# Kernel tuning notes

Measured on AMD Instinct MI355X. Metric: run time of the kernel, lower is better.

Reference implementation:

```python
import jax, jax.numpy as jnp
import numpy as np

D_MODEL = 512
D_STATE = 128
D_CONV = 4
EXPAND = 2
HEADDIM = 64
D_INNER = EXPAND * D_MODEL            # 1024
NHEADS = D_INNER // HEADDIM           # 16
CONV_DIM = D_INNER + 2 * D_STATE      # 1280
D_IN_PROJ = 2 * D_INNER + 2 * D_STATE + NHEADS  # 2320
EPS = 1e-5


def _mamba2(u, in_w, conv_w, conv_b, A_log, dt_bias, Dp, norm_w, out_w):
    # u: [b, l, d_model]  -- Mamba2 forward (ngroups=1), SSD in exact quadratic form
    b, l, _ = u.shape
    zxbcdt = u @ in_w.T                                   # [b,l,2320]
    z = zxbcdt[..., :D_INNER]
    xBC = zxbcdt[..., D_INNER:D_INNER + CONV_DIM]
    dt = zxbcdt[..., D_INNER + CONV_DIM:]                 # [b,l,nheads]
    # causal depthwise conv1d (kernel 4) + silu
    xp = jnp.pad(xBC, ((0, 0), (D_CONV - 1, 0), (0, 0)))
    conv = sum(xp[:, k:k + l, :] * conv_w[:, k] for k in range(D_CONV))
    xBC = jax.nn.silu(conv + conv_b)
    x = xBC[..., :D_INNER].reshape(b, l, NHEADS, HEADDIM)
    Bm = xBC[..., D_INNER:D_INNER + D_STATE]              # [b,l,d_state]
    Cm = xBC[..., D_INNER + D_STATE:]                     # [b,l,d_state]
    dt = jax.nn.softplus(dt + dt_bias)                    # [b,l,nheads]
    dtA = dt * (-jnp.exp(A_log))                          # [b,l,nheads], negative
    # SSD quadratic (semiseparable) form: L[t,s] = exp(sum_{r=s+1..t} dtA_r), causal
    cs = jnp.cumsum(dtA, axis=1)                          # [b,l,nh]
    seg = cs[:, :, None, :] - cs[:, None, :, :]           # [b,t,s,nh]
    mask = jnp.tril(jnp.ones((l, l), bool))
    L = jnp.exp(jnp.where(mask[None, :, :, None], seg, -jnp.inf))
    G = jnp.einsum('btd,bsd->bts', Cm, Bm)                # C_t . B_s
    dtx = dt[..., None] * x                               # [b,l,nh,hd]
    y = jnp.einsum('btsn,bsnp->btnp', G[..., None] * L, dtx)
    y = (y + x * Dp[:, None]).reshape(b, l, D_INNER)      # D skip
    # gated RMSNorm (norm_before_gate=False): rmsnorm(y * silu(z)) * weight
    y = y * jax.nn.silu(z)
    y = y * jax.lax.rsqrt(jnp.mean(jnp.square(y), -1, keepdims=True) + EPS) * norm_w
    return y @ out_w.T


def _forward(x, h_in_w, h_conv_w, h_conv_b, h_A_log, h_dt_bias, h_D, h_norm_w, h_out_w,
             v_in_w, v_conv_w, v_conv_b, v_A_log, v_dt_bias, v_D, v_norm_w, v_out_w,
             fc_w, fc_b):
    B, H, W, C = x.shape
    hp = (h_in_w, h_conv_w, h_conv_b, h_A_log, h_dt_bias, h_D, h_norm_w, h_out_w)
    vp = (v_in_w, v_conv_w, v_conv_b, v_A_log, v_dt_bias, v_D, v_norm_w, v_out_w)
    # horizontal: scan along W for each (B*H) row
    xh = x.reshape(-1, W, C)
    h1 = _mamba2(xh, *hp)
    # NOTE: original code flips dim 0 (batch), reproduced faithfully
    h2 = jnp.flip(_mamba2(jnp.flip(xh, 0), *hp), 0)
    h = jnp.concatenate([h1, h2], -1).reshape(B, H, W, -1)
    # vertical: scan along H for each (B*W) column
    xv = jnp.transpose(x, (0, 2, 1, 3)).reshape(-1, H, C)
    v1 = _mamba2(xv, *vp)
    v2 = jnp.flip(_mamba2(jnp.flip(xv, 0), *vp), 0)
    v = jnp.transpose(jnp.concatenate([v1, v2], -1).reshape(B, W, H, -1), (0, 2, 1, 3))
    out = jnp.concatenate([v, h], -1) @ fc_w.T + fc_b     # [B,H,W,C]
    return out


def setup_inputs() -> dict:
    key = jax.random.key(0)
    ks = jax.random.split(key, 8)
    B, H, W, C = 2, 64, 64, D_MODEL
    x = jax.random.normal(ks[0], (B, H, W, C), jnp.float32)

    def mk(k):
        kk = jax.random.split(k, 5)
        return {
            'in_w': 0.02 * jax.random.normal(kk[0], (D_IN_PROJ, D_MODEL), jnp.float32),
            'conv_w': 0.1 * jax.random.normal(kk[1], (CONV_DIM, D_CONV), jnp.float32),
            'conv_b': jnp.zeros((CONV_DIM,), jnp.float32),
            'A_log': jnp.log(jax.random.uniform(kk[2], (NHEADS,), jnp.float32, 1.0, 16.0)),
            'dt_bias': jnp.log(jnp.expm1(jax.random.uniform(kk[3], (NHEADS,), jnp.float32, 1e-3, 0.1))),
            'D': jnp.ones((NHEADS,), jnp.float32),
            'norm_w': jnp.ones((D_INNER,), jnp.float32),
            'out_w': 0.02 * jax.random.normal(kk[4], (D_MODEL, D_INNER), jnp.float32),
        }

    hp, vp = mk(ks[1]), mk(ks[2])
    inp = {'x': x}
    inp.update({f'h_{n}': v for n, v in hp.items()})
    inp.update({f'v_{n}': v for n, v in vp.items()})
    inp['fc_w'] = 0.02 * jax.random.normal(ks[3], (D_MODEL, 4 * D_MODEL), jnp.float32)
    inp['fc_b'] = jnp.zeros((D_MODEL,), jnp.float32)
    return inp


def reference(x, h_in_w, h_conv_w, h_conv_b, h_A_log, h_dt_bias, h_D, h_norm_w, h_out_w,
              v_in_w, v_conv_w, v_conv_b, v_A_log, v_dt_bias, v_D, v_norm_w, v_out_w,
              fc_w, fc_b):
    return _forward(x, h_in_w, h_conv_w, h_conv_b, h_A_log, h_dt_bias, h_D, h_norm_w, h_out_w,
                    v_in_w, v_conv_w, v_conv_b, v_A_log, v_dt_bias, v_D, v_norm_w, v_out_w,
                    fc_w, fc_b)
```

## Files before the change

### kernel.cpp

```cpp
#include <hip/hip_runtime.h>

#define NROWS 8192
#define NZX   2304
#define BCS   136
#define XMS   72

typedef __attribute__((ext_vector_type(8))) short bf16x8;
typedef __attribute__((ext_vector_type(4))) float f32x4;

__device__ __forceinline__ float bf2f(unsigned short u) {
    union { unsigned int i; float f; } v; v.i = ((unsigned int)u) << 16; return v.f;
}
__device__ __forceinline__ unsigned short f2bf(float f) {
    union { float f; unsigned int i; } v; v.f = f;
    unsigned int r = v.i + 0x7FFFu + ((v.i >> 16) & 1u);
    return (unsigned short)(r >> 16);
}

__device__ __forceinline__ void async_lds16(const unsigned short* g, unsigned short* l) {
    __builtin_amdgcn_global_load_lds(
        (const __attribute__((address_space(1))) unsigned int*)g,
        (__attribute__((address_space(3))) unsigned int*)l, 16, 0, 0);
}

__global__ void cvt_bf16(const float* __restrict__ s, unsigned short* __restrict__ d, int n4)
{
    int i = blockIdx.x * 256 + threadIdx.x;
    if (i >= n4) return;
    float4 v = *(const float4*)(s + (size_t)i * 4);
    ushort4 o;
    o.x = f2bf(v.x); o.y = f2bf(v.y); o.z = f2bf(v.z); o.w = f2bf(v.w);
    *(ushort4*)(d + (size_t)i * 4) = o;
}

__global__ void cvt2_bf16(const float* __restrict__ s0, const float* __restrict__ s1,
                          unsigned short* __restrict__ d, int n4)
{
    int i = blockIdx.x * 256 + threadIdx.x;
    if (i >= n4) return;
    const float* s = blockIdx.y ? s1 : s0;
    float4 v = *(const float4*)(s + (size_t)i * 4);
    ushort4 o;
    o.x = f2bf(v.x); o.y = f2bf(v.y); o.z = f2bf(v.z); o.w = f2bf(v.w);
    *(ushort4*)(d + (size_t)blockIdx.y * (2304 * 512) + (size_t)i * 4) = o;
}

__global__ __launch_bounds__(256) void cvtT_bf16(
    const float* __restrict__ s0, const float* __restrict__ s1,
    unsigned short* __restrict__ d0, unsigned short* __restrict__ d1)
{
    __shared__ float T[64][65];
    const float* s = blockIdx.z ? s1 : s0;
    unsigned short* d = blockIdx.z ? d1 : d0;
    const int tid = threadIdx.x;
    const int bo = blockIdx.x * 64, bc = blockIdx.y * 64;
#pragma unroll
    for (int i = 0; i < 16; ++i) {
        int slot = tid + i * 256;
        int r = slot >> 6, c = slot & 63;
        T[r][c] = s[(size_t)(bo + r) * 1024 + bc + c];
    }
    __syncthreads();
#pragma unroll
    for (int i = 0; i < 16; ++i) {
        int slot = tid + i * 256;
        int cr = slot >> 6, oc = slot & 63;
        d[(size_t)(bc + cr) * 512 + bo + oc] = f2bf(T[oc][cr]);
    }
}

__global__ __launch_bounds__(256) void gemm128_btz(
    const unsigned short* __restrict__ A0, const unsigned short* __restrict__ A1,
    const unsigned short* __restrict__ B0, const unsigned short* __restrict__ B1,
    unsigned short* __restrict__ C0, unsigned short* __restrict__ C1,
    int K, int lda, int ldb, int ldc, int permflag)
{
    __shared__ unsigned short As[128 * 32];
    __shared__ unsigned short Bs[128 * 32];
    const int z = blockIdx.z;
    const unsigned short* A = z ? A1 : A0;
    const unsigned short* B = z ? B1 : B0;
    unsigned short* C = z ? C1 : C0;
    const int perm = permflag & z;
    const int tid = threadIdx.x, wave = tid >> 6, lane = tid & 63;
    const int mB = blockIdx.x * 128, nB = blockIdx.y * 128;
    const int wm = (wave >> 1) * 64, wn = (wave & 1) * 64;
    const int lr = lane & 15, lq = lane >> 4;
    const int s0 = wave * 64 + lane, s1 = s0 + 256;
    const int row0 = s0 >> 2, q0 = (s0 & 3) ^ ((row0 >> 1) & 3);
    const int row1 = s1 >> 2, q1 = (s1 & 3) ^ ((row1 >> 1) & 3);
    int ar0 = mB + row0, ar1 = mB + row1;
    if (perm) {
        ar0 = (ar0 & ~4095) | ((ar0 & 63) << 6) | ((ar0 >> 6) & 63);
        ar1 = (ar1 & ~4095) | ((ar1 & 63) << 6) | ((ar1 >> 6) & 63);
    }
    const unsigned short* Ag0 = A + (size_t)ar0 * lda + q0 * 8;
    const unsigned short* Ag1 = A + (size_t)ar1 * lda + q1 * 8;
    const unsigned short* Bg0 = B + (size_t)(nB + row0) * ldb + q0 * 8;
    const unsigned short* Bg1 = B + (size_t)(nB + row1) * ldb + q1 * 8;
    unsigned short* lA0 = As + s0 * 8; unsigned short* lA1 = As + s1 * 8;
    unsigned short* lB0 = Bs + s0 * 8; unsigned short* lB1 = Bs + s1 * 8;
    const int sw = (lq ^ ((lr >> 1) & 3)) * 8;
    int aoff[4], boff[4];
#pragma unroll
    for (int i = 0; i < 4; ++i) {
        aoff[i] = (wm + i * 16 + lr) * 32 + sw;
        boff[i] = (wn + i * 16 + lr) * 32 + sw;
    }
    f32x4 zero4 = {0.f,0.f,0.f,0.f};
    f32x4 acc[4][4] = {{zero4,zero4,zero4,zero4},{zero4,zero4,zero4,zero4},
                       {zero4,zero4,zero4,zero4},{zero4,zero4,zero4,zero4}};
    for (int k0 = 0; k0 < K; k0 += 32) {
        async_lds16(Ag0 + k0, lA0);
        async_lds16(Ag1 + k0, lA1);
        async_lds16(Bg0 + k0, lB0);
        async_lds16(Bg1 + k0, lB1);
        __syncthreads();
        bf16x8 a[4], b[4];
#pragma unroll
        for (int i = 0; i < 4; ++i) a[i] = *(const bf16x8*)(As + aoff[i]);
#pragma unroll
        for (int i = 0; i < 4; ++i) b[i] = *(const bf16x8*)(Bs + boff[i]);
#pragma unroll
        for (int mi = 0; mi < 4; ++mi)
#pragma unroll
            for (int ni = 0; ni < 4; ++ni)
                acc[mi][ni] = __builtin_amdgcn_mfma_f32_16x16x32_bf16(
                    a[mi], b[ni], acc[mi][ni], 0, 0, 0);
        __syncthreads();
    }
    const int rbase = lq * 4;
#pragma unroll
    for (int mi = 0; mi < 4; ++mi)
#pragma unroll
        for (int ni = 0; ni < 4; ++ni) {
            int col = nB + wn + ni * 16 + lr;
#pragma unroll
            for (int r = 0; r < 4; ++r) {
                int row = mB + wm + mi * 16 + rbase + r;
                C[(size_t)row * ldc + col] = f2bf(acc[mi][ni][r]);
            }
        }
}

__global__ __launch_bounds__(256) void gemm_final2048(
    const unsigned short* __restrict__ YV, const unsigned short* __restrict__ YH,
    const unsigned short* __restrict__ W, const float* __restrict__ bias,
    float* __restrict__ C)
{
    __shared__ unsigned short As[128 * 32];
    __shared__ unsigned short Bs[64 * 32];
    const int tid = threadIdx.x, wave = tid >> 6, lane = tid & 63;
    const int mB = blockIdx.x * 128, nB = blockIdx.y * 64;
    const int lr = lane & 15, lq = lane >> 4;
    const int sA0 = tid, sA1 = tid + 256;
    const int rA0 = sA0 >> 2, qA0 = ((sA0 & 3) ^ ((rA0 >> 1) & 3)) * 8;
    const int rA1 = sA1 >> 2, qA1 = ((sA1 & 3) ^ ((rA1 >> 1) & 3)) * 8;
    const int rB  = tid >> 2, qB  = ((tid & 3) ^ ((rB >> 1) & 3)) * 8;
    const int g0r = mB + rA0, g1r = mB + rA1;
    const int p0r = (g0r & ~4095) | ((g0r & 63) << 6) | ((g0r >> 6) & 63);
    const int p1r = (g1r & ~4095) | ((g1r & 63) << 6) | ((g1r >> 6) & 63);
    const unsigned short* Bg = W + (size_t)(nB + rB) * 2048 + qB;
    unsigned short* lA0 = As + sA0 * 8; unsigned short* lA1 = As + sA1 * 8;
    unsigned short* lB  = Bs + tid * 8;
    const int sw = (lq ^ ((lr >> 1) & 3)) * 8;
    int aoff[2], boff[4];
#pragma unroll
    for (int i = 0; i < 2; ++i) aoff[i] = (wave * 32 + i * 16 + lr) * 32 + sw;
#pragma unroll
    for (int i = 0; i < 4; ++i) boff[i] = (i * 16 + lr) * 32 + sw;
    f32x4 zero4 = {0.f,0.f,0.f,0.f};
    f32x4 acc[2][4] = {{zero4,zero4,zero4,zero4},{zero4,zero4,zero4,zero4}};
    for (int k0 = 0; k0 < 2048; k0 += 32) {
        int kk0 = k0 + qA0, kk1 = k0 + qA1;
        const unsigned short* g0 = (kk0 < 1024) ? YV + (size_t)p0r * 1024 + kk0
                                                : YH + (size_t)g0r * 1024 + (kk0 - 1024);
        const unsigned short* g1 = (kk1 < 1024) ? YV + (size_t)p1r * 1024 + kk1
                                                : YH + (size_t)g1r * 1024 + (kk1 - 1024);
        async_lds16(g0, lA0);
        async_lds16(g1, lA1);
        async_lds16(Bg + k0, lB);
        __syncthreads();
        bf16x8 a[2], b[4];
#pragma unroll
        for (int i = 0; i < 2; ++i) a[i] = *(const bf16x8*)(As + aoff[i]);
#pragma unroll
        for (int i = 0; i < 4; ++i) b[i] = *(const bf16x8*)(Bs + boff[i]);
#pragma unroll
        for (int mi = 0; mi < 2; ++mi)
#pragma unroll
            for (int ni = 0; ni < 4; ++ni)
                acc[mi][ni] = __builtin_amdgcn_mfma_f32_16x16x32_bf16(
                    a[mi], b[ni], acc[mi][ni], 0, 0, 0);
        __syncthreads();
    }
    const int rbase = lq * 4;
#pragma unroll
    for (int mi = 0; mi < 2; ++mi)
#pragma unroll
        for (int ni = 0; ni < 4; ++ni) {
            int col = nB + ni * 16 + lr;
            float bb = bias[col];
#pragma unroll
            for (int r = 0; r < 4; ++r) {
                int row = mB + wave * 32 + mi * 16 + rbase + r;
                C[(size_t)row * 512 + col] = acc[mi][ni][r] + bb;
            }
        }
}

__global__ __launch_bounds__(320) void conv_silu(
    const unsigned short* __restrict__ zxb, const float* __restrict__ cw0,
    const float* __restrict__ cw1, const float* __restrict__ cb0,
    const float* __restrict__ cb1, unsigned short* __restrict__ xbcb)
{
    __shared__ unsigned short S[64 * 320];
    const int dir = blockIdx.y;
    const unsigned short* zx = zxb + (size_t)dir * NROWS * NZX;
    unsigned short* xbc = xbcb + (size_t)dir * NROWS * 1280;
    const float* cw = dir ? cw1 : cw0;
    const float* cb = dir ? cb1 : cb0;
    const int tid = threadIdx.x;
    const int seq = blockIdx.x >> 2, tile = blockIdx.x & 3;
    const int cbase = tile * 320;
    const unsigned short* src = zx + (size_t)seq * 64 * NZX + 1024 + cbase;
#pragma unroll
    for (int i = 0; i < 8; ++i) {
        int slot = tid + i * 320;
        int r = slot / 40, ch = (slot % 40) * 8;
        *(uint4*)(S + r * 320 + ch) = *(const uint4*)(src + (size_t)r * NZX + ch);
    }
    __syncthreads();
    const int c8 = (tid % 40) * 8, rg = tid / 40;
    const int gc = cbase + c8;
    float4 b0 = *(const float4*)(cb + gc), b1 = *(const float4*)(cb + gc + 4);
    const float bias[8] = {b0.x,b0.y,b0.z,b0.w,b1.x,b1.y,b1.z,b1.w};
    float4 wv[8];
#pragma unroll
    for (int j = 0; j < 8; ++j) wv[j] = *(const float4*)(cw + (size_t)(gc + j) * 4);
    unsigned short* dst = xbc + (size_t)seq * 64 * 1280 + gc;
#pragma unroll
    for (int r = 0; r < 8; ++r) {
        int t = rg * 8 + r;
        float acc[8];
#pragma unroll
        for (int j = 0; j < 8; ++j) acc[j] = bias[j];
#pragma unroll
        for (int k = 0; k < 4; ++k) {
            int ts = t + k - 3;
            if (ts >= 0) {
                uint4 xv = *(const uint4*)(S + ts * 320 + c8);
                const unsigned short* xs = (const unsigned short*)&xv;
#pragma unroll
                for (int j = 0; j < 8; ++j)
                    acc[j] += bf2f(xs[j]) * ((const float*)&wv[j])[k];
            }
        }
        unsigned short out8[8] __attribute__((aligned(16)));
#pragma unroll
        for (int j = 0; j < 8; ++j) out8[j] = f2bf(acc[j] / (1.f + __expf(-acc[j])));
        *(uint4*)(dst + (size_t)t * 1280) = *(const uint4*)out8;
    }
}

__global__ __launch_bounds__(256) void dt_cs(
    const float* __restrict__ x, const float* __restrict__ iw0,
    const float* __restrict__ iw1, const float* __restrict__ db0,
    const float* __restrict__ db1, const float* __restrict__ al0,
    const float* __restrict__ al1, float* __restrict__ dtbb,
    float* __restrict__ csbb)
{
    __shared__ float wsm[4][512];
    __shared__ float xs[64][68];
    __shared__ float dta[4][64], dtt[4][64];
    const int dir = blockIdx.y;
    const float* in_w = dir ? iw1 : iw0;
    const float* dt_bias = dir ? db1 : db0;
    const float* A_log = dir ? al1 : al0;
    float* dtb = dtbb + (size_t)dir * 131072;
    float* csb = csbb + (size_t)dir * 131072;
    const int tid = threadIdx.x;
    const int seq = blockIdx.x >> 2, hq = blockIdx.x & 3;
#pragma unroll
    for (int i = 0; i < 2; ++i) {
        int slot = tid + i * 256;
        int h = slot >> 7, c = (slot & 127) * 4;
        *(float4*)&wsm[h][c] = *(const float4*)(in_w + (size_t)(2304 + hq * 4 + h) * 512 + c);
    }
    const int t = tid & 63, hh = tid >> 6;
    const int h = hq * 4 + hh;
    float acc = 0.f;
    for (int c0 = 0; c0 < 512; c0 += 64) {
        __syncthreads();
#pragma unroll
        for (int i = 0; i < 4; ++i) {
            int slot = tid + i * 256;
            int r = slot >> 4, cc = (slot & 15) * 4;
            size_t row = (dir == 0) ? (size_t)seq * 64 + r
                                    : (size_t)(seq >> 6) * 4096 + (size_t)r * 64 + (seq & 63);
            *(float4*)&xs[r][cc] = *(const float4*)(x + row * 512 + c0 + cc);
        }
        __syncthreads();
#pragma unroll
        for (int cc = 0; cc < 64; cc += 4) {
            float4 u4 = *(const float4*)&xs[t][cc];
            const float* w = &wsm[hh][c0 + cc];
            acc += u4.x * w[0] + u4.y * w[1] + u4.z * w[2] + u4.w * w[3];
        }
    }
    float v = acc + dt_bias[h];
    float dtv = (v > 20.f) ? v : log1pf(__expf(v));
    dtt[hh][t] = dtv;
    dta[hh][t] = dtv * -__expf(A_log[h]);
    __syncthreads();
    if (tid < 4) {
        float run = 0.f;
        int ob = (seq * 16 + hq * 4 + tid) * 64;
        for (int tt = 0; tt < 64; ++tt) {
            run += dta[tid][tt];
            dtb[ob + tt] = dtt[tid][tt];
            csb[ob + tt] = run;
        }
    }
}

__global__ __launch_bounds__(256) void scan_kernel(
    const unsigned short* __restrict__ xbcb, const float* __restrict__ dtbb,
    const float* __restrict__ csbb, const float* __restrict__ Dv0,
    const float* __restrict__ Dv1, unsigned short* __restrict__ yh,
    unsigned short* __restrict__ yv)
{
    __shared__ unsigned short Bs[64 * BCS];
    __shared__ unsigned short Cs[64 * BCS];
    __shared__ unsigned short XsT[64 * XMS];
    __shared__ unsigned short Ms[64 * XMS];
    __shared__ float dts[64], css[64];
    const int dir = blockIdx.y;
    const unsigned short* xbc = xbcb + (size_t)dir * NROWS * 1280;
    const float* dtb = dtbb + (size_t)dir * 131072;
    const float* csb = csbb + (size_t)dir * 131072;
    const float* Dv = dir ? Dv1 : Dv0;
    unsigned short* y = dir ? yv : yh;
    const int tid = threadIdx.x;
    const int lane = tid & 63, wave = tid >> 6;
    const int seq = blockIdx.x >> 4, h = blockIdx.x & 15;
    if (tid < 64) {
        dts[tid] = dtb[(seq * 16 + h) * 64 + tid];
        css[tid] = csb[(seq * 16 + h) * 64 + tid];
    }
    const unsigned short* base = xbc + (size_t)seq * 64 * 1280;
#pragma unroll
    for (int i = 0; i < 4; ++i) {
        int e = (tid + i * 256) * 8;
        int r = e >> 7, c = e & 127;
        *(uint4*)(Bs + r * BCS + c) = *(const uint4*)(base + (size_t)r * 1280 + 1024 + c);
        *(uint4*)(Cs + r * BCS + c) = *(const uint4*)(base + (size_t)r * 1280 + 1152 + c);
    }
#pragma unroll
    for (int i = 0; i < 2; ++i) {
        int e = (tid + i * 256) * 8;
        int t = e >> 6, p0 = e & 63;
        uint4 xval = *(const uint4*)(base + (size_t)t * 1280 + h * 64 + p0);
        const unsigned short* xs = (const unsigned short*)&xval;
#pragma unroll
        for (int j = 0; j < 8; ++j) {
            int jl = (j + lane) & 7;
            XsT[(p0 + jl) * XMS + t] = xs[jl];
        }
    }
    __syncthreads();
    const int lr = lane & 15, lq = lane >> 4;
    f32x4 zero4 = {0.f,0.f,0.f,0.f};
    f32x4 acc[4] = {zero4, zero4, zero4, zero4};
#pragma unroll
    for (int kt = 0; kt < 4; ++kt) {
        bf16x8 a = *(const bf16x8*)(Cs + (wave * 16 + lr) * BCS + kt * 32 + lq * 8);
#pragma unroll
        for (int ni = 0; ni < 4; ++ni) {
            bf16x8 b = *(const bf16x8*)(Bs + (ni * 16 + lr) * BCS + kt * 32 + lq * 8);
            acc[ni] = __builtin_amdgcn_mfma_f32_16x16x32_bf16(a, b, acc[ni], 0, 0, 0);
        }
    }
    float css_t[4];
#pragma unroll
    for (int r = 0; r < 4; ++r) css_t[r] = css[wave * 16 + lq * 4 + r];
#pragma unroll
    for (int ni = 0; ni < 4; ++ni) {
        int s = ni * 16 + lr;
        float cs_s = css[s], dt_s = dts[s];
#pragma unroll
        for (int r = 0; r < 4; ++r) {
            int t = wave * 16 + lq * 4 + r;
            float e = __expf(fminf(css_t[r] - cs_s, 0.f));
            float m = (s <= t) ? acc[ni][r] * e * dt_s : 0.f;
            Ms[t * XMS + s] = f2bf(m);
        }
    }
    __syncthreads();
    f32x4 yacc[4] = {zero4, zero4, zero4, zero4};
#pragma unroll
    for (int kt = 0; kt < 2; ++kt) {
        bf16x8 a = *(const bf16x8*)(Ms + (wave * 16 + lr) * XMS + kt * 32 + lq * 8);
#pragma unroll
        for (int ni = 0; ni < 4; ++ni) {
            bf16x8 b = *(const bf16x8*)(XsT + (ni * 16 + lr) * XMS + kt * 32 + lq * 8);
            yacc[ni] = __builtin_amdgcn_mfma_f32_16x16x32_bf16(a, b, yacc[ni], 0, 0, 0);
        }
    }
    const float Dh = Dv[h];
    unsigned short* yout = y + (size_t)seq * 64 * 1024 + h * 64;
#pragma unroll
    for (int ni = 0; ni < 4; ++ni) {
        int p = ni * 16 + lr;
#pragma unroll
        for (int r = 0; r < 4; ++r) {
            int t = wave * 16 + lq * 4 + r;
            float v = yacc[ni][r] + Dh * bf2f(XsT[p * XMS + t]);
            yout[(size_t)t * 1024 + p] = f2bf(v);
        }
    }
}

__global__ __launch_bounds__(128) void gate_norm(
    const unsigned short* __restrict__ zxb, unsigned short* __restrict__ yh,
    unsigned short* __restrict__ yv, const float* __restrict__ nw0,
    const float* __restrict__ nw1)
{
    const int dir = blockIdx.y;
    const unsigned short* zx = zxb + (size_t)dir * NROWS * NZX;
    unsigned short* y = dir ? yv : yh;
    const float* nw = dir ? nw1 : nw0;
    const int row = blockIdx.x, tid = threadIdx.x;
    uint4 yv4 = *(const uint4*)(y + (size_t)row * 1024 + tid * 8);
    uint4 zv4 = *(const uint4*)(zx + (size_t)row * NZX + tid * 8);
    const unsigned short* ys = (const unsigned short*)&yv4;
    const unsigned short* zs = (const unsigned short*)&zv4;
    float g[8]; float ss = 0.f;
#pragma unroll
    for (int j = 0; j < 8; ++j) {
        float zv = bf2f(zs[j]);
        float gv = bf2f(ys[j]) * (zv / (1.f + __expf(-zv)));
        g[j] = gv; ss += gv * gv;
    }
#pragma unroll
    for (int off = 32; off > 0; off >>= 1) ss += __shfl_xor(ss, off, 64);
    __shared__ float red[2];
    if ((tid & 63) == 0) red[tid >> 6] = ss;
    __syncthreads();
    ss = red[0] + red[1];
    const float scale = rsqrtf(ss * (1.f / 1024.f) + 1e-5f);
    unsigned short out8[8] __attribute__((aligned(16)));
#pragma unroll
    for (int j = 0; j < 8; ++j) out8[j] = f2bf(g[j] * scale * nw[tid * 8 + j]);
    *(uint4*)(y + (size_t)row * 1024 + tid * 8) = *(const uint4*)out8;
}

__global__ void fold_w(const float* __restrict__ fcw, unsigned short* __restrict__ wf)
{
    int idx = blockIdx.x * 256 + threadIdx.x;
    if (idx >= 512 * 1024) return;
    int o = idx >> 10, c = idx & 1023;
    int half = c >> 9, cc = c & 511;
    float v = fcw[(size_t)o * 2048 + half * 1024 + cc] +
              fcw[(size_t)o * 2048 + half * 1024 + 512 + cc];
    wf[idx] = f2bf(v);
}

extern "C" void kernel_launch(void* const* d_in, const int* in_sizes, int n_in,
                              void* d_out, int out_size, void* d_ws, size_t ws_size,
                              hipStream_t stream)
{
    (void)in_sizes; (void)n_in; (void)out_size; (void)ws_size;
    const float* x   = (const float*)d_in[0];
    const float* fcw = (const float*)d_in[17];
    const float* fcb = (const float*)d_in[18];
    const float* iw0 = (const float*)d_in[1];  const float* iw1 = (const float*)d_in[9];
    const float* cw0 = (const float*)d_in[2];  const float* cw1 = (const float*)d_in[10];
    const float* cb0 = (const float*)d_in[3];  const float* cb1 = (const float*)d_in[11];
    const float* al0 = (const float*)d_in[4];  const float* al1 = (const float*)d_in[12];
    const float* db0 = (const float*)d_in[5];  const float* db1 = (const float*)d_in[13];
    const float* Dv0 = (const float*)d_in[6];  const float* Dv1 = (const float*)d_in[14];
    const float* nw0 = (const float*)d_in[7];  const float* nw1 = (const float*)d_in[15];
    const float* ow0 = (const float*)d_in[8];  const float* ow1 = (const float*)d_in[16];

    char* ws = (char*)d_ws;
    size_t off = 0;
    auto alloc = [&](size_t bytes) {
        void* p = ws + off; off += (bytes + 255) & ~(size_t)255; return p;
    };
    unsigned short* xbf   = (unsigned short*)alloc((size_t)NROWS * 512 * 2);
    unsigned short* wbA   = (unsigned short*)alloc((size_t)2 * 2304 * 512 * 2);
    unsigned short* wbOT0 = (unsigned short*)alloc((size_t)1024 * 512 * 2);
    unsigned short* wbOT1 = (unsigned short*)alloc((size_t)1024 * 512 * 2);
    unsigned short* wf    = (unsigned short*)alloc((size_t)512 * 1024 * 2);
    unsigned short* wcomb = (unsigned short*)alloc((size_t)512 * 2048 * 2);
    unsigned short* zx    = (unsigned short*)alloc((size_t)2 * NROWS * NZX * 2);
    unsigned short* xbc   = (unsigned short*)alloc((size_t)2 * NROWS * 1280 * 2);
    float* dtb            = (float*)alloc((size_t)2 * 2048 * 64 * 4);
    float* csb            = (float*)alloc((size_t)2 * 2048 * 64 * 4);
    unsigned short* ybh   = (unsigned short*)alloc((size_t)NROWS * 1024 * 2);
    unsigned short* ybv   = (unsigned short*)alloc((size_t)NROWS * 1024 * 2);

    cvt_bf16<<<(NROWS * 512 / 4 + 255) / 256, 256, 0, stream>>>(x, xbf, NROWS * 512 / 4);
    fold_w<<<(512 * 1024) / 256, 256, 0, stream>>>(fcw, wf);
    cvt2_bf16<<<dim3(1152, 2), 256, 0, stream>>>(iw0, iw1, wbA, 2304 * 512 / 4);
    cvtT_bf16<<<dim3(8, 16, 2), 256, 0, stream>>>(ow0, ow1, wbOT0, wbOT1);
    gemm128_btz<<<dim3(4, 8, 2), 256, 0, stream>>>(
        wf + 512, wf, wbOT0, wbOT1, wcomb + 1024, wcomb, 512, 1024, 512, 2048, 0);

    gemm128_btz<<<dim3(64, 18, 2), 256, 0, stream>>>(
        xbf, xbf, wbA, wbA + 2304 * 512, zx, zx + (size_t)NROWS * NZX,
        512, 512, 512, NZX, 1);
    conv_silu<<<dim3(512, 2), 320, 0, stream>>>(zx, cw0, cw1, cb0, cb1, xbc);
    dt_cs<<<dim3(512, 2), 256, 0, stream>>>(x, iw0, iw1, db0, db1, al0, al1, dtb, csb);
    scan_kernel<<<dim3(2048, 2), 256, 0, stream>>>(xbc, dtb, csb, Dv0, Dv1, ybh, ybv);
    gate_norm<<<dim3(NROWS, 2), 128, 0, stream>>>(zx, ybh, ybv, nw0, nw1);
    gemm_final2048<<<dim3(64, 8), 256, 0, stream>>>(ybv, ybh, wcomb, fcb, (float*)d_out);
}
```

Measured before the change: 314.9 us.

## Merge prep kernels and GEMMs into fewer launches, stage GEMM stores via LDS

Folds the conversion, weight-fold, transpose and dt/cumsum kernels into one block-dispatched prep kernel. The two GEMM launches (weight combine and input projection) become a single grid. This cuts launch count and inter-kernel gaps. The GEMM epilogue now writes bf16 results through a swizzled LDS tile so global stores are 16-byte vectors instead of scattered 2-byte stores. The bf16 rounding also drops round-to-even for simple round-half-up, which slightly changes numerics.

```diff
diff --git a/kernel.cpp b/kernel.cpp
--- a/kernel.cpp
+++ b/kernel.cpp
@@ -5,6 +5,12 @@
 #define BCS   136
 #define XMS   72
 
+#define PB0 4096
+#define PB1 (PB0 + 2048)
+#define PB2 (PB1 + 2304)
+#define PB3 (PB2 + 256)
+#define PB4 (PB3 + 1024)
+
 typedef __attribute__((ext_vector_type(8))) short bf16x8;
 typedef __attribute__((ext_vector_type(4))) float f32x4;
 
@@ -13,8 +19,7 @@
 }
 __device__ __forceinline__ unsigned short f2bf(float f) {
     union { float f; unsigned int i; } v; v.f = f;
-    unsigned int r = v.i + 0x7FFFu + ((v.i >> 16) & 1u);
-    return (unsigned short)(r >> 16);
+    return (unsigned short)((v.i + 0x8000u) >> 16);
 }
 
 __device__ __forceinline__ void async_lds16(const unsigned short* g, unsigned short* l) {
@@ -23,67 +28,144 @@
         (__attribute__((address_space(3))) unsigned int*)l, 16, 0, 0);
 }
 
-__global__ void cvt_bf16(const float* __restrict__ s, unsigned short* __restrict__ d, int n4)
-{
-    int i = blockIdx.x * 256 + threadIdx.x;
-    if (i >= n4) return;
-    float4 v = *(const float4*)(s + (size_t)i * 4);
-    ushort4 o;
-    o.x = f2bf(v.x); o.y = f2bf(v.y); o.z = f2bf(v.z); o.w = f2bf(v.w);
-    *(ushort4*)(d + (size_t)i * 4) = o;
-}
-
-__global__ void cvt2_bf16(const float* __restrict__ s0, const float* __restrict__ s1,
-                          unsigned short* __restrict__ d, int n4)
-{
-    int i = blockIdx.x * 256 + threadIdx.x;
-    if (i >= n4) return;
-    const float* s = blockIdx.y ? s1 : s0;
-    float4 v = *(const float4*)(s + (size_t)i * 4);
-    ushort4 o;
-    o.x = f2bf(v.x); o.y = f2bf(v.y); o.z = f2bf(v.z); o.w = f2bf(v.w);
-    *(ushort4*)(d + (size_t)blockIdx.y * (2304 * 512) + (size_t)i * 4) = o;
-}
-
-__global__ __launch_bounds__(256) void cvtT_bf16(
-    const float* __restrict__ s0, const float* __restrict__ s1,
-    unsigned short* __restrict__ d0, unsigned short* __restrict__ d1)
-{
-    __shared__ float T[64][65];
-    const float* s = blockIdx.z ? s1 : s0;
-    unsigned short* d = blockIdx.z ? d1 : d0;
-    const int tid = threadIdx.x;
-    const int bo = blockIdx.x * 64, bc = blockIdx.y * 64;
-#pragma unroll
-    for (int i = 0; i < 16; ++i) {
-        int slot = tid + i * 256;
-        int r = slot >> 6, c = slot & 63;
-        T[r][c] = s[(size_t)(bo + r) * 1024 + bc + c];
-    }
-    __syncthreads();
-#pragma unroll
-    for (int i = 0; i < 16; ++i) {
-        int slot = tid + i * 256;
-        int cr = slot >> 6, oc = slot & 63;
-        d[(size_t)(bc + cr) * 512 + bo + oc] = f2bf(T[oc][cr]);
-    }
-}
-
-__global__ __launch_bounds__(256) void gemm128_btz(
-    const unsigned short* __restrict__ A0, const unsigned short* __restrict__ A1,
-    const unsigned short* __restrict__ B0, const unsigned short* __restrict__ B1,
-    unsigned short* __restrict__ C0, unsigned short* __restrict__ C1,
-    int K, int lda, int ldb, int ldc, int permflag)
-{
-    __shared__ unsigned short As[128 * 32];
-    __shared__ unsigned short Bs[128 * 32];
-    const int z = blockIdx.z;
-    const unsigned short* A = z ? A1 : A0;
-    const unsigned short* B = z ? B1 : B0;
-    unsigned short* C = z ? C1 : C0;
-    const int perm = permflag & z;
+__global__ __launch_bounds__(256) void prep_kernel(
+    const float* __restrict__ x, const float* __restrict__ fcw,
+    const float* __restrict__ iw0, const float* __restrict__ iw1,
+    const float* __restrict__ ow0, const float* __restrict__ ow1,
+    const float* __restrict__ db0, const float* __restrict__ db1,
+    const float* __restrict__ al0, const float* __restrict__ al1,
+    unsigned short* __restrict__ xbf, unsigned short* __restrict__ wf,
+    unsigned short* __restrict__ wbA, unsigned short* __restrict__ wbOT0,
+    unsigned short* __restrict__ wbOT1, float* __restrict__ dtbb,
+    float* __restrict__ csbb)
+{
+    __shared__ char sm[27648] __attribute__((aligned(16)));
+    const int blk = blockIdx.x, tid = threadIdx.x;
+    if (blk < PB0) {
+        int i = blk * 256 + tid;
+        float4 v = *(const float4*)(x + (size_t)i * 4);
+        ushort4 o;
+        o.x = f2bf(v.x); o.y = f2bf(v.y); o.z = f2bf(v.z); o.w = f2bf(v.w);
+        *(ushort4*)(xbf + (size_t)i * 4) = o;
+    } else if (blk < PB1) {
+        int idx = (blk - PB0) * 256 + tid;
+        int o = idx >> 10, c = idx & 1023;
+        int half = c >> 9, cc = c & 511;
+        float v = fcw[(size_t)o * 2048 + half * 1024 + cc] +
+                  fcw[(size_t)o * 2048 + half * 1024 + 512 + cc];
+        wf[idx] = f2bf(v);
+    } else if (blk < PB2) {
+        int local = blk - PB1;
+        int dir = local / 1152;
+        int i = (local % 1152) * 256 + tid;
+        const float* s = dir ? iw1 : iw0;
+        float4 v = *(const float4*)(s + (size_t)i * 4);
+        ushort4 o;
+        o.x = f2bf(v.x); o.y = f2bf(v.y); o.z = f2bf(v.z); o.w = f2bf(v.w);
+        *(ushort4*)(wbA + (size_t)dir * (2304 * 512) + (size_t)i * 4) = o;
+    } else if (blk < PB3) {
+        float (*T)[65] = (float(*)[65])sm;
+        int local = blk - PB2;
+        int z = local >> 7, rem = local & 127;
+        const float* s = z ? ow1 : ow0;
+        unsigned short* d = z ? wbOT1 : wbOT0;
+        const int bo = (rem >> 4) * 64, bc = (rem & 15) * 64;
+#pragma unroll
+        for (int i = 0; i < 16; ++i) {
+            int slot = tid + i * 256;
+            int r = slot >> 6, c = slot & 63;
+            T[r][c] = s[(size_t)(bo + r) * 1024 + bc + c];
+        }
+        __syncthreads();
+#pragma unroll
+        for (int i = 0; i < 16; ++i) {
+            int slot = tid + i * 256;
+            int cr = slot >> 6, oc = slot & 63;
+            d[(size_t)(bc + cr) * 512 + bo + oc] = f2bf(T[oc][cr]);
+        }
+    } else {
+        float (*wsm)[512] = (float(*)[512])sm;
+        float (*xs)[68]   = (float(*)[68])(sm + 8192);
+        float (*dta)[64]  = (float(*)[64])(sm + 8192 + 17408);
+        float (*dtt)[64]  = (float(*)[64])(sm + 8192 + 17408 + 1024);
+        int local = blk - PB3;
+        const int dir = local >> 9, bxl = local & 511;
+        const float* in_w = dir ? iw1 : iw0;
+        const float* dt_bias = dir ? db1 : db0;
+        const float* A_log = dir ? al1 : al0;
+        float* dtb = dtbb + (size_t)dir * 131072;
+        float* csb = csbb + (size_t)dir * 131072;
+        const int seq = bxl >> 2, hq = bxl & 3;
+#pragma unroll
+        for (int i = 0; i < 2; ++i) {
+            int slot = tid + i * 256;
+            int h = slot >> 7, c = (slot & 127) * 4;
+            *(float4*)&wsm[h][c] = *(const float4*)(in_w + (size_t)(2304 + hq * 4 + h) * 512 + c);
+        }
+        const int t = tid & 63, hh = tid >> 6;
+        const int h = hq * 4 + hh;
+        float acc = 0.f;
+        for (int c0 = 0; c0 < 512; c0 += 64) {
+            __syncthreads();
+#pragma unroll
+            for (int i = 0; i < 4; ++i) {
+                int slot = tid + i * 256;
+                int r = slot >> 4, cc = (slot & 15) * 4;
+                size_t row = (dir == 0) ? (size_t)seq * 64 + r
+                                        : (size_t)(seq >> 6) * 4096 + (size_t)r * 64 + (seq & 63);
+                *(float4*)&xs[r][cc] = *(const float4*)(x + row * 512 + c0 + cc);
+            }
+            __syncthreads();
+#pragma unroll
+            for (int cc = 0; cc < 64; cc += 4) {
+                float4 u4 = *(const float4*)&xs[t][cc];
+                const float* w = &wsm[hh][c0 + cc];
+                acc += u4.x * w[0] + u4.y * w[1] + u4.z * w[2] + u4.w * w[3];
+            }
+        }
+        float v = acc + dt_bias[h];
+        float dtv = (v > 20.f) ? v : log1pf(__expf(v));
+        dtt[hh][t] = dtv;
+        dta[hh][t] = dtv * -__expf(A_log[h]);
+        __syncthreads();
+        if (tid < 4) {
+            float run = 0.f;
+            int ob = (seq * 16 + hq * 4 + tid) * 64;
+            for (int tt = 0; tt < 64; ++tt) {
+                run += dta[tid][tt];
+                dtb[ob + tt] = dtt[tid][tt];
+                csb[ob + tt] = run;
+            }
+        }
+    }
+}
+
+__global__ __launch_bounds__(256) void gemm_phase(
+    const unsigned short* __restrict__ xbf, const unsigned short* __restrict__ wbA,
+    unsigned short* __restrict__ zx, const unsigned short* __restrict__ wf,
+    const unsigned short* __restrict__ wbOT0, const unsigned short* __restrict__ wbOT1,
+    unsigned short* __restrict__ wcomb)
+{
+    __shared__ unsigned short SMEM[8192];
+    unsigned short* As = SMEM;
+    unsigned short* Bs = SMEM + 4096;
+    const int bx = blockIdx.x, by = blockIdx.y, z = blockIdx.z;
+    const unsigned short *A, *B;
+    unsigned short* C;
+    int lda, ldb, ldc, perm, mB, nB;
+    if (bx < 64) {
+        A = xbf; lda = 512; perm = z;
+        B = wbA + (size_t)z * (2304 * 512); ldb = 512;
+        C = zx + (size_t)z * NROWS * NZX; ldc = NZX;
+        mB = bx * 128; nB = by * 128;
+    } else {
+        if (by >= 8) return;
+        A = z ? wf : wf + 512; lda = 1024; perm = 0;
+        B = z ? wbOT1 : wbOT0; ldb = 512;
+        C = z ? wcomb : wcomb + 1024; ldc = 2048;
+        mB = (bx - 64) * 128; nB = by * 128;
+    }
     const int tid = threadIdx.x, wave = tid >> 6, lane = tid & 63;
-    const int mB = blockIdx.x * 128, nB = blockIdx.y * 128;
     const int wm = (wave >> 1) * 64, wn = (wave & 1) * 64;
     const int lr = lane & 15, lq = lane >> 4;
     const int s0 = wave * 64 + lane, s1 = s0 + 256;
@@ -110,7 +192,7 @@
     f32x4 zero4 = {0.f,0.f,0.f,0.f};
     f32x4 acc[4][4] = {{zero4,zero4,zero4,zero4},{zero4,zero4,zero4,zero4},
                        {zero4,zero4,zero4,zero4},{zero4,zero4,zero4,zero4}};
-    for (int k0 = 0; k0 < K; k0 += 32) {
+    for (int k0 = 0; k0 < 512; k0 += 32) {
         async_lds16(Ag0 + k0, lA0);
         async_lds16(Ag1 + k0, lA1);
         async_lds16(Bg0 + k0, lB0);
@@ -129,18 +211,29 @@
                     a[mi], b[ni], acc[mi][ni], 0, 0, 0);
         __syncthreads();
     }
-    const int rbase = lq * 4;
-#pragma unroll
-    for (int mi = 0; mi < 4; ++mi)
+    unsigned short* WR = SMEM + wave * 1024;
+#pragma unroll
+    for (int mi = 0; mi < 4; ++mi) {
 #pragma unroll
         for (int ni = 0; ni < 4; ++ni) {
-            int col = nB + wn + ni * 16 + lr;
 #pragma unroll
             for (int r = 0; r < 4; ++r) {
-                int row = mB + wm + mi * 16 + rbase + r;
-                C[(size_t)row * ldc + col] = f2bf(acc[mi][ni][r]);
+                int r16 = lq * 4 + r;
+                int cn = ni * 16 + lr;
+                int gp = ((cn >> 3) + (r16 >> 1)) & 7;
+                WR[r16 * 64 + gp * 8 + (cn & 7)] = f2bf(acc[mi][ni][r]);
             }
         }
+#pragma unroll
+        for (int j = 0; j < 2; ++j) {
+            int r16 = j * 8 + (lane >> 3);
+            int gr = lane & 7;
+            int gp = (gr + (r16 >> 1)) & 7;
+            uint4 v = *(const uint4*)(WR + r16 * 64 + gp * 8);
+            int row = mB + wm + mi * 16 + r16;
+            *(uint4*)(C + (size_t)row * ldc + nB + wn + gr * 8) = v;
+        }
+    }
 }
 
 __global__ __launch_bounds__(256) void gemm_final2048(
@@ -263,67 +356,6 @@
     }
 }
 
-__global__ __launch_bounds__(256) void dt_cs(
-    const float* __restrict__ x, const float* __restrict__ iw0,
-    const float* __restrict__ iw1, const float* __restrict__ db0,
-    const float* __restrict__ db1, const float* __restrict__ al0,
-    const float* __restrict__ al1, float* __restrict__ dtbb,
-    float* __restrict__ csbb)
-{
-    __shared__ float wsm[4][512];
-    __shared__ float xs[64][68];
-    __shared__ float dta[4][64], dtt[4][64];
-    const int dir = blockIdx.y;
-    const float* in_w = dir ? iw1 : iw0;
-    const float* dt_bias = dir ? db1 : db0;
-    const float* A_log = dir ? al1 : al0;
-    float* dtb = dtbb + (size_t)dir * 131072;
-    float* csb = csbb + (size_t)dir * 131072;
-    const int tid = threadIdx.x;
-    const int seq = blockIdx.x >> 2, hq = blockIdx.x & 3;
-#pragma unroll
-    for (int i = 0; i < 2; ++i) {
-        int slot = tid + i * 256;
-        int h = slot >> 7, c = (slot & 127) * 4;
-        *(float4*)&wsm[h][c] = *(const float4*)(in_w + (size_t)(2304 + hq * 4 + h) * 512 + c);
-    }
-    const int t = tid & 63, hh = tid >> 6;
-    const int h = hq * 4 + hh;
-    float acc = 0.f;
-    for (int c0 = 0; c0 < 512; c0 += 64) {
-        __syncthreads();
-#pragma unroll
-        for (int i = 0; i < 4; ++i) {
-            int slot = tid + i * 256;
-            int r = slot >> 4, cc = (slot & 15) * 4;
-            size_t row = (dir == 0) ? (size_t)seq * 64 + r
-                                    : (size_t)(seq >> 6) * 4096 + (size_t)r * 64 + (seq & 63);
-            *(float4*)&xs[r][cc] = *(const float4*)(x + row * 512 + c0 + cc);
-        }
-        __syncthreads();
-#pragma unroll
-        for (int cc = 0; cc < 64; cc += 4) {
-            float4 u4 = *(const float4*)&xs[t][cc];
-            const float* w = &wsm[hh][c0 + cc];
-            acc += u4.x * w[0] + u4.y * w[1] + u4.z * w[2] + u4.w * w[3];
-        }
-    }
-    float v = acc + dt_bias[h];
-    float dtv = (v > 20.f) ? v : log1pf(__expf(v));
-    dtt[hh][t] = dtv;
-    dta[hh][t] = dtv * -__expf(A_log[h]);
-    __syncthreads();
-    if (tid < 4) {
-        float run = 0.f;
-        int ob = (seq * 16 + hq * 4 + tid) * 64;
-        for (int tt = 0; tt < 64; ++tt) {
-            run += dta[tid][tt];
-            dtb[ob + tt] = dtt[tid][tt];
-            csb[ob + tt] = run;
-        }
-    }
-}
-
 __global__ __launch_bounds__(256) void scan_kernel(
     const unsigned short* __restrict__ xbcb, const float* __restrict__ dtbb,
     const float* __restrict__ csbb, const float* __restrict__ Dv0,
@@ -455,17 +487,6 @@
     *(uint4*)(y + (size_t)row * 1024 + tid * 8) = *(const uint4*)out8;
 }
 
-__global__ void fold_w(const float* __restrict__ fcw, unsigned short* __restrict__ wf)
-{
-    int idx = blockIdx.x * 256 + threadIdx.x;
-    if (idx >= 512 * 1024) return;
-    int o = idx >> 10, c = idx & 1023;
-    int half = c >> 9, cc = c & 511;
-    float v = fcw[(size_t)o * 2048 + half * 1024 + cc] +
-              fcw[(size_t)o * 2048 + half * 1024 + 512 + cc];
-    wf[idx] = f2bf(v);
-}
-
 extern "C" void kernel_launch(void* const* d_in, const int* in_sizes, int n_in,
                               void* d_out, int out_size, void* d_ws, size_t ws_size,
                               hipStream_t stream)
@@ -501,18 +522,12 @@
     unsigned short* ybh   = (unsigned short*)alloc((size_t)NROWS * 1024 * 2);
     unsigned short* ybv   = (unsigned short*)alloc((size_t)NROWS * 1024 * 2);
 
-    cvt_bf16<<<(NROWS * 512 / 4 + 255) / 256, 256, 0, stream>>>(x, xbf, NROWS * 512 / 4);
-    fold_w<<<(512 * 1024) / 256, 256, 0, stream>>>(fcw, wf);
-    cvt2_bf16<<<dim3(1152, 2), 256, 0, stream>>>(iw0, iw1, wbA, 2304 * 512 / 4);
-    cvtT_bf16<<<dim3(8, 16, 2), 256, 0, stream>>>(ow0, ow1, wbOT0, wbOT1);
-    gemm128_btz<<<dim3(4, 8, 2), 256, 0, stream>>>(
-        wf + 512, wf, wbOT0, wbOT1, wcomb + 1024, wcomb, 512, 1024, 512, 2048, 0);
-
-    gemm128_btz<<<dim3(64, 18, 2), 256, 0, stream>>>(
-        xbf, xbf, wbA, wbA + 2304 * 512, zx, zx + (size_t)NROWS * NZX,
-        512, 512, 512, NZX, 1);
+    prep_kernel<<<PB4, 256, 0, stream>>>(x, fcw, iw0, iw1, ow0, ow1, db0, db1,
+                                         al0, al1, xbf, wf, wbA, wbOT0, wbOT1,
+                                         dtb, csb);
+    gemm_phase<<<dim3(68, 18, 2), 256, 0, stream>>>(xbf, wbA, zx, wf,
+                                                    wbOT0, wbOT1, wcomb);
     conv_silu<<<dim3(512, 2), 320, 0, stream>>>(zx, cw0, cw1, cb0, cb1, xbc);
-    dt_cs<<<dim3(512, 2), 256, 0, stream>>>(x, iw0, iw1, db0, db1, al0, al1, dtb, csb);
     scan_kernel<<<dim3(2048, 2), 256, 0, stream>>>(xbc, dtb, csb, Dv0, Dv1, ybh, ybv);
     gate_norm<<<dim3(NROWS, 2), 128, 0, stream>>>(zx, ybh, ybv, nw0, nw1);
     gemm_final2048<<<dim3(64, 8), 256, 0, stream>>>(ybv, ybh, wcomb, fcb, (float*)d_out);
```

Result: no change. 309.2 us (-1.8%).
